# Performance work log

Hardware: AMD Instinct MI355X
Metric: run time of the kernel (lower is better)

Reference implementation:

```python
import jax, jax.numpy as jnp
import numpy as np

IMAGE_C = 1
IMAGE_W = 28
PIXELS_PER_ROW = IMAGE_W * IMAGE_C  # 28

B, T, E = 16, IMAGE_W * IMAGE_W * IMAGE_C, 512  # T = 784
H = 8
D = E // H  # head_dim = 64


def get_2d_causal_bias(T):
    idx = jnp.arange(T)
    i = idx // PIXELS_PER_ROW          # row index
    j = (idx % PIXELS_PER_ROW) // IMAGE_C  # col index
    c = idx % IMAGE_C                  # channel index
    q_i, k_i = i[:, None], i[None, :]
    q_j, k_j = j[:, None], j[None, :]
    q_c, k_c = c[:, None], c[None, :]
    allowed = (k_i < q_i) | ((k_i == q_i) & (k_j < q_j)) | (
        (k_i == q_i) & (k_j == q_j) & (k_c <= q_c))
    bias = jnp.where(allowed, 0.0, -jnp.inf).astype(jnp.float32)
    return bias[None, None]  # [1, 1, T, T]


def setup_inputs() -> dict:
    key = jax.random.key(0)
    ks = jax.random.split(key, 5)
    s = 1.0 / np.sqrt(E)
    return {
        "x": jax.random.normal(ks[0], (B, T, E), dtype=jnp.float32),
        "Wq": jax.random.normal(ks[1], (E, E), dtype=jnp.float32) * s,
        "bq": jnp.zeros((E,), dtype=jnp.float32),
        "Wk": jax.random.normal(ks[2], (E, E), dtype=jnp.float32) * s,
        "bk": jnp.zeros((E,), dtype=jnp.float32),
        "Wv": jax.random.normal(ks[3], (E, E), dtype=jnp.float32) * s,
        "bv": jnp.zeros((E,), dtype=jnp.float32),
        "Wo": jax.random.normal(ks[4], (E, E), dtype=jnp.float32) * s,
        "bo": jnp.zeros((E,), dtype=jnp.float32),
    }


def reference(x, Wq, bq, Wk, bk, Wv, bv, Wo, bo):
    Bx, Tx, Ex = x.shape
    # projections (torch Linear: y = x @ W.T + b; here W stored as [E, E] used directly)
    Q = (x @ Wq + bq).reshape(Bx, Tx, H, D).transpose(0, 2, 1, 3)  # [B,H,T,D]
    K = (x @ Wk + bk).reshape(Bx, Tx, H, D).transpose(0, 2, 1, 3)
    V = (x @ Wv + bv).reshape(Bx, Tx, H, D).transpose(0, 2, 1, 3)
    scores = jnp.einsum("bhqd,bhkd->bhqk", Q, K) / jnp.sqrt(jnp.float32(D))
    scores = scores + get_2d_causal_bias(Tx)
    attn = jax.nn.softmax(scores, axis=-1)
    ctx = jnp.einsum("bhqk,bhkd->bhqd", attn, V)
    ctx = ctx.transpose(0, 2, 1, 3).reshape(Bx, Tx, Ex)
    return ctx @ Wo + bo
```

## Files before the change

kernel.cpp:

```cpp
#include <hip/hip_runtime.h>
#include <hip/hip_bf16.h>

#define BB    16
#define TT    784
#define TPK   832
#define TPQ   896
#define EE    512
#define HH    8
#define DD    64
#define BT    (BB*TT)

typedef short short8 __attribute__((ext_vector_type(8)));
typedef short short4v __attribute__((ext_vector_type(4)));
typedef float floatx4 __attribute__((ext_vector_type(4)));
typedef float floatx16 __attribute__((ext_vector_type(16)));
typedef unsigned uint4v __attribute__((ext_vector_type(4)));

__device__ __forceinline__ short f2bf(float f) {
    unsigned u = __builtin_bit_cast(unsigned, f);
    u += 0x7FFFu + ((u >> 16) & 1u);
    return (short)(u >> 16);
}

__device__ __forceinline__ unsigned cvtpk_bf16(float lo, float hi) {
    unsigned r;
    asm("v_cvt_pk_bf16_f32 %0, %1, %2" : "=v"(r) : "v"(lo), "v"(hi));
    return r;
}

__device__ __forceinline__ void gload_lds16(const short* g, short* l) {
    __builtin_amdgcn_global_load_lds(
        (const __attribute__((address_space(1))) void*)g,
        (__attribute__((address_space(3))) void*)l, 16, 0, 0);
}

__global__ void prep_kernel(const float* __restrict__ x, short* __restrict__ xb,
                            const float* __restrict__ Wq, const float* __restrict__ Wk,
                            const float* __restrict__ Wv, short* __restrict__ wqkvt,
                            const float* __restrict__ Wo, short* __restrict__ wot,
                            short* __restrict__ Qb, short* __restrict__ Kb, short* __restrict__ Vt)
{
    __shared__ short t[64][65];
    int b = blockIdx.x;
    if (b < 3136) {
        int i = (b * 256 + threadIdx.x) * 8;
        float4 a = *(const float4*)(x + i);
        float4 c = *(const float4*)(x + i + 4);
        short8 o;
        o[0] = f2bf(a.x); o[1] = f2bf(a.y); o[2] = f2bf(a.z); o[3] = f2bf(a.w);
        o[4] = f2bf(c.x); o[5] = f2bf(c.y); o[6] = f2bf(c.z); o[7] = f2bf(c.w);
        *(short8*)(xb + i) = o;
    } else if (b < 3392) {
        const float* W; short* out; int n0, k0;
        if (b < 3328) {
            int tt = b - 3136;
            n0 = (tt % 24) * 64; k0 = (tt / 24) * 64;
            W = (n0 < 512) ? Wq : (n0 < 1024 ? Wk : Wv);
            out = wqkvt;
        } else {
            int tt = b - 3328;
            n0 = (tt % 8) * 64; k0 = (tt / 8) * 64;
            W = Wo; out = wot;
        }
        int nn0 = n0 & 511;
        for (int i = threadIdx.x; i < 4096; i += 256) {
            int r = i >> 6, c = i & 63;
            t[r][c] = f2bf(W[(k0 + r) * 512 + nn0 + c]);
        }
        __syncthreads();
        for (int i = threadIdx.x; i < 4096; i += 256) {
            int nr = i >> 6, kc = i & 63;
            out[(n0 + nr) * 512 + k0 + kc] = t[kc][nr];
        }
    } else {
        int c = (b - 3392) * 256 + threadIdx.x;
        short8 z = (short8){0,0,0,0,0,0,0,0};
        if (c < 114688) {
            int bh = c / 896, j = c - bh * 896;
            *(short8*)&Qb[(bh * TPQ + TT) * 64 + j * 8] = z;
        } else if (c < 163840) {
            int c2 = c - 114688;
            int bh = c2 / 384, j = c2 - bh * 384;
            *(short8*)&Kb[(bh * TPK + TT) * 64 + j * 8] = z;
        } else {
            int c3 = c - 163840;
            int bh = c3 / 384, j = c3 - bh * 384;
            int d = j / 6, m = j - d * 6;
            *(short8*)&Vt[(bh * 64 + d) * TPK + TT + m * 8] = z;
        }
    }
}

__global__ __launch_bounds__(256, 4) void gemm_qkv_kernel(
    const short* __restrict__ A, const short* __restrict__ Bt,
    const float* __restrict__ bq, const float* __restrict__ bk, const float* __restrict__ bv,
    short* __restrict__ Qb, short* __restrict__ Kb, short* __restrict__ Vt)
{
    __shared__ __align__(16) short smem[16640];
    short* As0 = smem;
    short* Bs0 = smem + 8192;

    const int orig = blockIdx.x;
    const int tile = (orig & 7) * 147 + (orig >> 3);
    const int m0 = (tile / 12) * 128, n0 = (tile % 12) * 128;
    const int tid = threadIdx.x;
    const int lane = tid & 63, w = tid >> 6;
    const int wr = w >> 1, wc = w & 1;
    const int l16 = lane & 15, quad = lane >> 4;

    const int srow = w * 32 + (lane >> 2);
    const int scol = (lane & 3) * 8;
    const short* Ag = A  + (size_t)(m0 + srow) * 512 + scol;
    const short* Bg = Bt + (size_t)(n0 + srow) * 512 + scol;
    short* Abase = As0 + w * 1024;
    short* Bbase = Bs0 + w * 1024;

    auto stage = [&](int it) {
        int b = it & 1;
        int ko = it * 32;
        gload_lds16(Ag + ko,            Abase + b * 4096);
        gload_lds16(Ag + ko + 16 * 512, Abase + b * 4096 + 512);
        gload_lds16(Bg + ko,            Bbase + b * 4096);
        gload_lds16(Bg + ko + 16 * 512, Bbase + b * 4096 + 512);
    };

    floatx4 acc[4][4];
    #pragma unroll
    for (int i = 0; i < 4; i++)
        #pragma unroll
        for (int j = 0; j < 4; j++)
            acc[i][j] = (floatx4){0.f, 0.f, 0.f, 0.f};

    stage(0);
    __syncthreads();

    for (int it = 0; it < 16; it++) {
        if (it < 15) stage(it + 1);
        const short* as = As0 + (it & 1) * 4096;
        const short* bs = Bs0 + (it & 1) * 4096;
        short8 af[4], bf[4];
        #pragma unroll
        for (int i = 0; i < 4; i++) {
            af[i] = *(const short8*)&as[(wr * 64 + i * 16 + l16) * 32 + quad * 8];
            bf[i] = *(const short8*)&bs[(wc * 64 + i * 16 + l16) * 32 + quad * 8];
        }
        #pragma unroll
        for (int mi = 0; mi < 4; mi++)
            #pragma unroll
            for (int ni = 0; ni < 4; ni++)
                acc[mi][ni] = __builtin_amdgcn_mfma_f32_16x16x32_bf16(af[mi], bf[ni], acc[mi][ni], 0, 0, 0);
        __syncthreads();
    }

    const int sel = n0 >> 9;
    if (sel == 2) {
        #pragma unroll
        for (int mi = 0; mi < 4; mi++) {
            int m = m0 + wr * 64 + mi * 16 + quad * 4;
            int bb = m / TT, t = m - bb * TT;
            #pragma unroll
            for (int ni = 0; ni < 4; ni++) {
                int nn = (n0 + wc * 64 + ni * 16 + l16) & 511;
                int hh = nn >> 6, dd = nn & 63;
                float b = bv[nn];
                short4v pv;
                #pragma unroll
                for (int r = 0; r < 4; r++) pv[r] = f2bf(acc[mi][ni][r] + b);
                *(short4v*)&Vt[((size_t)(bb * HH + hh) * 64 + dd) * TPK + t] = pv;
            }
        }
    } else {
        short* Ct = smem;
        const float* bias = (sel == 0) ? bq : bk;
        #pragma unroll
        for (int mi = 0; mi < 4; mi++) {
            #pragma unroll
            for (int ni = 0; ni < 4; ni++) {
                int nl = wc * 64 + ni * 16 + l16;
                int nn = (n0 + nl) & 511;
                float b = bias[nn];
                #pragma unroll
                for (int r = 0; r < 4; r++) {
                    float v = acc[mi][ni][r] + b;
                    if (sel == 0) v *= 0.125f;
                    Ct[(wr * 64 + mi * 16 + quad * 4 + r) * 130 + nl] = f2bf(v);
                }
            }
        }
        __syncthreads();
        short* dst = (sel == 0) ? Qb : Kb;
        const int tp = (sel == 0) ? TPQ : TPK;
        int nl = lane * 2;
        int nn = (n0 + nl) & 511;
        int hh = nn >> 6, dd = nn & 63;
        #pragma unroll 4
        for (int rr = 0; rr < 32; rr++) {
            int ml = w * 32 + rr;
            int m = m0 + ml;
            int bb = m / TT, t = m - bb * TT;
            unsigned pv = *(const unsigned*)&Ct[ml * 130 + nl];
            *(unsigned*)&dst[((bb * HH + hh) * tp + t) * 64 + dd] = pv;
        }
    }
}

__global__ __launch_bounds__(256, 3) void attn_kernel(
    const short* __restrict__ Qb, const short* __restrict__ Kb, const short* __restrict__ Vt,
    short* __restrict__ ctx)
{
    const int g = blockIdx.x;
    const int low = g & 7, rest = g >> 3;
    const int qb = 6 - (rest >> 4);
    const int bh = ((rest & 15) << 3) | low;
    const int bb = bh >> 3, hh = bh & 7;
    const int tid = threadIdx.x;
    const int lane = tid & 63, w = tid >> 6;
    const int l32 = lane & 31, hi = lane >> 5;
    const int r7 = l32 & 7;

    __shared__ __align__(16) short Ks[2][4096];
    __shared__ __align__(16) short Vs[2][4096];

    const short* Kbase = Kb + (size_t)(bh * TPK) * 64;
    const short* Vbase = Vt + (size_t)(bh * 64) * TPK;

    const int srow = tid >> 3;
    const int sc8  = tid & 7;
    const int scol = sc8 * 8;
    const int ksw  = (sc8 ^ (srow & 7)) * 8;
    const int vg0  = (sc8 >> 1) * 2;
    const int vsw0 = ((vg0       ^ (srow & 7)) * 8) + (sc8 & 1) * 4;
    const int vsw1 = (((vg0 + 1) ^ (srow & 7)) * 8) + (sc8 & 1) * 4;

    short8 kreg[2], vreg[2];
    auto load_tile = [&](int kt) {
        #pragma unroll
        for (int p = 0; p < 2; p++) {
            int row = srow + p * 32;
            kreg[p] = *(const short8*)(Kbase + (kt * 64 + row) * 64 + scol);
            vreg[p] = *(const short8*)(Vbase + row * TPK + kt * 64 + scol);
        }
    };
    auto store_tile = [&](int b) {
        #pragma unroll
        for (int p = 0; p < 2; p++) {
            int ro = (srow + p * 32) * 64;
            *(short8*)&Ks[b][ro + ksw] = kreg[p];
            short4v v0, v1;
            #pragma unroll
            for (int i = 0; i < 4; i++) { v0[i] = vreg[p][i]; v1[i] = vreg[p][i + 4]; }
            *(short4v*)&Vs[b][ro + vsw0] = v0;
            *(short4v*)&Vs[b][ro + vsw1] = v1;
        }
    };

    const int q0   = qb * 128;
    const int q_lo = q0 + w * 32;
    const int qg   = q_lo + l32;
    const bool wreal = (q_lo < TT);
    const int q_top = (q0 + 127 < TT - 1) ? (q0 + 127) : (TT - 1);
    const int KT = (q_top >> 6) + 1;

    const short* Qrow = Qb + (size_t)(bh * TPQ + qg) * 64;
    short8 qf[4];
    #pragma unroll
    for (int d = 0; d < 4; d++) qf[d] = *(const short8*)(Qrow + d * 16 + hi * 8);

    floatx16 accO[2];
    #pragma unroll
    for (int dt = 0; dt < 2; dt++)
        #pragma unroll
        for (int i = 0; i < 16; i++) accO[dt][i] = 0.f;
    float accL = 0.f;

    load_tile(0);
    store_tile(0);

    for (int kt = 0; kt < KT; kt++) {
        const int cb = kt & 1;
        if (kt < KT - 1) load_tile(kt + 1);
        __syncthreads();
        if (wreal) {
            #pragma unroll
            for (int kh = 0; kh < 2; kh++) {
                const int kbase = kt * 64 + kh * 32;
                if (kbase > q_lo + 31) continue;
                floatx16 z;
                #pragma unroll
                for (int i = 0; i < 16; i++) z[i] = 0.f;
                #pragma unroll
                for (int d = 0; d < 4; d++) {
                    short8 kf = *(const short8*)&Ks[cb][(kh * 32 + l32) * 64 + (((d * 2 + hi) ^ r7) * 8)];
                    z = __builtin_amdgcn_mfma_f32_32x32x16_bf16(kf, qf[d], z, 0, 0, 0);
                }
                float p[16];
                #pragma unroll
                for (int r = 0; r < 16; r++) p[r] = __expf(z[r]);
                if (kbase + 31 > q_lo) {
                    #pragma unroll
                    for (int r = 0; r < 16; r++) {
                        int keyg = kbase + (r & 3) + 8 * (r >> 2) + 4 * hi;
                        if (keyg > qg) p[r] = 0.f;
                    }
                }
                #pragma unroll
                for (int r = 0; r < 16; r++) accL += p[r];
                #pragma unroll
                for (int s = 0; s < 2; s++) {
                    uint4v pw;
                    #pragma unroll
                    for (int jj = 0; jj < 4; jj++)
                        pw[jj] = cvtpk_bf16(p[8 * s + 2 * jj], p[8 * s + 2 * jj + 1]);
                    short8 pb = __builtin_bit_cast(short8, pw);
                    #pragma unroll
                    for (int dt = 0; dt < 2; dt++) {
                        short8 vf = *(const short8*)&Vs[cb][(dt * 32 + l32) * 64 + (((kh * 4 + s * 2 + hi) ^ r7) * 8)];
                        accO[dt] = __builtin_amdgcn_mfma_f32_32x32x16_bf16(vf, pb, accO[dt], 0, 0, 0);
                    }
                }
            }
        }
        if (kt < KT - 1) store_tile((kt + 1) & 1);
    }

    float Lt = accL + __shfl_xor(accL, 32, 64);
    if (wreal && qg < TT) {
        float inv = 1.f / Lt;
        short* crow = ctx + (size_t)(bb * TT + qg) * 512 + hh * 64;
        #pragma unroll
        for (int dt = 0; dt < 2; dt++)
            #pragma unroll
            for (int g4 = 0; g4 < 4; g4++) {
                short4v pv;
                #pragma unroll
                for (int r4 = 0; r4 < 4; r4++) pv[r4] = f2bf(accO[dt][g4 * 4 + r4] * inv);
                *(short4v*)&crow[dt * 32 + g4 * 8 + 4 * hi] = pv;
            }
    }
}

__global__ __launch_bounds__(256, 4) void gemm_out_kernel(
    const short* __restrict__ A, const short* __restrict__ Bt,
    const float* __restrict__ bo, float* __restrict__ out)
{
    __shared__ __align__(16) short smem[16384];
    short* As0 = smem;
    short* Bs0 = smem + 8192;

    const int orig = blockIdx.x;
    const int tile = (orig & 7) * 49 + (orig >> 3);
    const int m0 = (tile >> 2) * 128, n0 = (tile & 3) * 128;
    const int tid = threadIdx.x;
    const int lane = tid & 63, w = tid >> 6;
    const int wr = w >> 1, wc = w & 1;
    const int l16 = lane & 15, quad = lane >> 4;

    const int srow = w * 32 + (lane >> 2);
    const int scol = (lane & 3) * 8;
    const short* Ag = A  + (size_t)(m0 + srow) * 512 + scol;
    const short* Bg = Bt + (size_t)(n0 + srow) * 512 + scol;
    short* Abase = As0 + w * 1024;
    short* Bbase = Bs0 + w * 1024;

    auto stage = [&](int it) {
        int b = it & 1;
        int ko = it * 32;
        gload_lds16(Ag + ko,            Abase + b * 4096);
        gload_lds16(Ag + ko + 16 * 512, Abase + b * 4096 + 512);
        gload_lds16(Bg + ko,            Bbase + b * 4096);
        gload_lds16(Bg + ko + 16 * 512, Bbase + b * 4096 + 512);
    };

    floatx4 acc[4][4];
    #pragma unroll
    for (int i = 0; i < 4; i++)
        #pragma unroll
        for (int j = 0; j < 4; j++)
            acc[i][j] = (floatx4){0.f, 0.f, 0.f, 0.f};

    stage(0);
    __syncthreads();

    for (int it = 0; it < 16; it++) {
        if (it < 15) stage(it + 1);
        const short* as = As0 + (it & 1) * 4096;
        const short* bs = Bs0 + (it & 1) * 4096;
        short8 af[4], bf[4];
        #pragma unroll
        for (int i = 0; i < 4; i++) {
            af[i] = *(const short8*)&as[(wr * 64 + i * 16 + l16) * 32 + quad * 8];
            bf[i] = *(const short8*)&bs[(wc * 64 + i * 16 + l16) * 32 + quad * 8];
        }
        #pragma unroll
        for (int mi = 0; mi < 4; mi++)
            #pragma unroll
            for (int ni = 0; ni < 4; ni++)
                acc[mi][ni] = __builtin_amdgcn_mfma_f32_16x16x32_bf16(af[mi], bf[ni], acc[mi][ni], 0, 0, 0);
        __syncthreads();
    }

    #pragma unroll
    for (int mi = 0; mi < 4; mi++) {
        #pragma unroll
        for (int ni = 0; ni < 4; ni++) {
            int n = n0 + wc * 64 + ni * 16 + l16;
            float bias = bo[n];
            #pragma unroll
            for (int r = 0; r < 4; r++) {
                int m = m0 + wr * 64 + mi * 16 + quad * 4 + r;
                out[(size_t)m * 512 + n] = acc[mi][ni][r] + bias;
            }
        }
    }
}

extern "C" void kernel_launch(void* const* d_in, const int* in_sizes, int n_in,
                              void* d_out, int out_size, void* d_ws, size_t ws_size,
                              hipStream_t stream) {
    const float* x  = (const float*)d_in[0];
    const float* Wq = (const float*)d_in[1];
    const float* bq = (const float*)d_in[2];
    const float* Wk = (const float*)d_in[3];
    const float* bk = (const float*)d_in[4];
    const float* Wv = (const float*)d_in[5];
    const float* bv = (const float*)d_in[6];
    const float* Wo = (const float*)d_in[7];
    const float* bo = (const float*)d_in[8];
    float* out = (float*)d_out;

    char* ws = (char*)d_ws;
    size_t off = 0;
    auto alloc = [&](size_t bytes) -> void* {
        void* p = ws + off;
        off += (bytes + 255) & ~(size_t)255;
        return p;
    };
    short* xb    = (short*)alloc((size_t)BT * EE * 2);
    short* wqkvt = (short*)alloc((size_t)1536 * 512 * 2);
    short* wot   = (short*)alloc((size_t)512 * 512 * 2);
    short* Qb    = (short*)alloc((size_t)BB * HH * TPQ * DD * 2);
    short* Kb    = (short*)alloc((size_t)BB * HH * TPK * DD * 2);
    short* Vtb   = (short*)alloc((size_t)BB * HH * DD * TPK * 2);
    short* ctxb  = (short*)alloc((size_t)BT * EE * 2);

    prep_kernel<<<4224, 256, 0, stream>>>(x, xb, Wq, Wk, Wv, wqkvt, Wo, wot, Qb, Kb, Vtb);
    gemm_qkv_kernel<<<1176, 256, 0, stream>>>(xb, wqkvt, bq, bk, bv, Qb, Kb, Vtb);
    attn_kernel<<<896, 256, 0, stream>>>(Qb, Kb, Vtb, ctxb);
    gemm_out_kernel<<<392, 256, 0, stream>>>(ctxb, wot, bo, out);
}
```

Baseline: 158.1 us.

## Reorganize GEMM LDS layout by k-chunk and halve out-proj M tile

The QKV and output GEMMs now store LDS tiles k-chunk-major (each 8-element k slice holds all rows contiguously). Each lane's short8 fragment read is then a contiguous row-stride-8 access, meant to avoid bank conflicts from the old 32-element row stride. The output projection also switches from 128x128 to 64x128 tiles with 784 blocks instead of 392, to fill more CUs on the small GEMM. The cost is less reuse per block and more redundant B loads.

```diff
diff --git a/kernel.cpp b/kernel.cpp
--- a/kernel.cpp
+++ b/kernel.cpp
@@ -108,20 +108,20 @@
     const int wr = w >> 1, wc = w & 1;
     const int l16 = lane & 15, quad = lane >> 4;
 
-    const int srow = w * 32 + (lane >> 2);
-    const int scol = (lane & 3) * 8;
-    const short* Ag = A  + (size_t)(m0 + srow) * 512 + scol;
-    const short* Bg = Bt + (size_t)(n0 + srow) * 512 + scol;
-    short* Abase = As0 + w * 1024;
-    short* Bbase = Bs0 + w * 1024;
+    const int sr = tid & 127;
+    const int sc = tid >> 7;
+    const short* Ag = A  + (size_t)(m0 + sr) * 512 + sc * 8;
+    const short* Bg = Bt + (size_t)(n0 + sr) * 512 + sc * 8;
+    short* Alb = As0 + w * 512;
+    short* Blb = Bs0 + w * 512;
 
     auto stage = [&](int it) {
         int b = it & 1;
         int ko = it * 32;
-        gload_lds16(Ag + ko,            Abase + b * 4096);
-        gload_lds16(Ag + ko + 16 * 512, Abase + b * 4096 + 512);
-        gload_lds16(Bg + ko,            Bbase + b * 4096);
-        gload_lds16(Bg + ko + 16 * 512, Bbase + b * 4096 + 512);
+        gload_lds16(Ag + ko,      Alb + b * 4096);
+        gload_lds16(Ag + ko + 16, Alb + b * 4096 + 2048);
+        gload_lds16(Bg + ko,      Blb + b * 4096);
+        gload_lds16(Bg + ko + 16, Blb + b * 4096 + 2048);
     };
 
     floatx4 acc[4][4];
@@ -141,8 +141,8 @@
         short8 af[4], bf[4];
         #pragma unroll
         for (int i = 0; i < 4; i++) {
-            af[i] = *(const short8*)&as[(wr * 64 + i * 16 + l16) * 32 + quad * 8];
-            bf[i] = *(const short8*)&bs[(wc * 64 + i * 16 + l16) * 32 + quad * 8];
+            af[i] = *(const short8*)&as[quad * 1024 + (wr * 64 + i * 16 + l16) * 8];
+            bf[i] = *(const short8*)&bs[quad * 1024 + (wc * 64 + i * 16 + l16) * 8];
         }
         #pragma unroll
         for (int mi = 0; mi < 4; mi++)
@@ -343,37 +343,34 @@
     const short* __restrict__ A, const short* __restrict__ Bt,
     const float* __restrict__ bo, float* __restrict__ out)
 {
-    __shared__ __align__(16) short smem[16384];
+    __shared__ __align__(16) short smem[12288];
     short* As0 = smem;
-    short* Bs0 = smem + 8192;
+    short* Bs0 = smem + 4096;
 
     const int orig = blockIdx.x;
-    const int tile = (orig & 7) * 49 + (orig >> 3);
-    const int m0 = (tile >> 2) * 128, n0 = (tile & 3) * 128;
+    const int tile = (orig & 7) * 98 + (orig >> 3);
+    const int m0 = (tile >> 2) * 64, n0 = (tile & 3) * 128;
     const int tid = threadIdx.x;
     const int lane = tid & 63, w = tid >> 6;
-    const int wr = w >> 1, wc = w & 1;
+    const int wm = w >> 1, wn = w & 1;
     const int l16 = lane & 15, quad = lane >> 4;
 
-    const int srow = w * 32 + (lane >> 2);
-    const int scol = (lane & 3) * 8;
-    const short* Ag = A  + (size_t)(m0 + srow) * 512 + scol;
-    const short* Bg = Bt + (size_t)(n0 + srow) * 512 + scol;
-    short* Abase = As0 + w * 1024;
-    short* Bbase = Bs0 + w * 1024;
+    const short* Ag = A + (size_t)(m0 + lane) * 512 + w * 8;
+    const short* Bg = Bt + (size_t)(n0 + (w & 1) * 64 + lane) * 512 + (w >> 1) * 8;
+    short* Alb = As0 + w * 512;
+    short* Blb = Bs0 + w * 512;
 
     auto stage = [&](int it) {
         int b = it & 1;
         int ko = it * 32;
-        gload_lds16(Ag + ko,            Abase + b * 4096);
-        gload_lds16(Ag + ko + 16 * 512, Abase + b * 4096 + 512);
-        gload_lds16(Bg + ko,            Bbase + b * 4096);
-        gload_lds16(Bg + ko + 16 * 512, Bbase + b * 4096 + 512);
+        gload_lds16(Ag + ko,      Alb + b * 2048);
+        gload_lds16(Bg + ko,      Blb + b * 4096);
+        gload_lds16(Bg + ko + 16, Blb + b * 4096 + 2048);
     };
 
-    floatx4 acc[4][4];
+    floatx4 acc[2][4];
     #pragma unroll
-    for (int i = 0; i < 4; i++)
+    for (int i = 0; i < 2; i++)
         #pragma unroll
         for (int j = 0; j < 4; j++)
             acc[i][j] = (floatx4){0.f, 0.f, 0.f, 0.f};
@@ -383,16 +380,17 @@
 
     for (int it = 0; it < 16; it++) {
         if (it < 15) stage(it + 1);
-        const short* as = As0 + (it & 1) * 4096;
+        const short* as = As0 + (it & 1) * 2048;
         const short* bs = Bs0 + (it & 1) * 4096;
-        short8 af[4], bf[4];
-        #pragma unroll
-        for (int i = 0; i < 4; i++) {
-            af[i] = *(const short8*)&as[(wr * 64 + i * 16 + l16) * 32 + quad * 8];
-            bf[i] = *(const short8*)&bs[(wc * 64 + i * 16 + l16) * 32 + quad * 8];
-        }
-        #pragma unroll
-        for (int mi = 0; mi < 4; mi++)
+        short8 af[2], bf[4];
+        #pragma unroll
+        for (int i = 0; i < 2; i++)
+            af[i] = *(const short8*)&as[quad * 512 + (wm * 32 + i * 16 + l16) * 8];
+        #pragma unroll
+        for (int j = 0; j < 4; j++)
+            bf[j] = *(const short8*)&bs[quad * 1024 + (wn * 64 + j * 16 + l16) * 8];
+        #pragma unroll
+        for (int mi = 0; mi < 2; mi++)
             #pragma unroll
             for (int ni = 0; ni < 4; ni++)
                 acc[mi][ni] = __builtin_amdgcn_mfma_f32_16x16x32_bf16(af[mi], bf[ni], acc[mi][ni], 0, 0, 0);
@@ -400,14 +398,14 @@
     }
 
     #pragma unroll
-    for (int mi = 0; mi < 4; mi++) {
+    for (int mi = 0; mi < 2; mi++) {
         #pragma unroll
         for (int ni = 0; ni < 4; ni++) {
-            int n = n0 + wc * 64 + ni * 16 + l16;
+            int n = n0 + wn * 64 + ni * 16 + l16;
             float bias = bo[n];
             #pragma unroll
             for (int r = 0; r < 4; r++) {
-                int m = m0 + wr * 64 + mi * 16 + quad * 4 + r;
+                int m = m0 + wm * 32 + mi * 16 + quad * 4 + r;
                 out[(size_t)m * 512 + n] = acc[mi][ni][r] + bias;
             }
         }
@@ -446,5 +444,5 @@
     prep_kernel<<<4224, 256, 0, stream>>>(x, xb, Wq, Wk, Wv, wqkvt, Wo, wot, Qb, Kb, Vtb);
     gemm_qkv_kernel<<<1176, 256, 0, stream>>>(xb, wqkvt, bq, bk, bv, Qb, Kb, Vtb);
     attn_kernel<<<896, 256, 0, stream>>>(Qb, Kb, Vtb, ctxb);
-    gemm_out_kernel<<<392, 256, 0, stream>>>(ctxb, wot, bo, out);
-}
+    gemm_out_kernel<<<784, 256, 0, stream>>>(ctxb, wot, bo, out);
+}
```

Result: slower. 188.2 us (+19.0%).
